# Kernel tuning notes

Hardware: AMD Instinct MI355X
Metric: run time of the kernel (lower is better)

## Reference

```python
import jax, jax.numpy as jnp
import numpy as np

# ---- hyperparams from init_kwargs ----
WX, WY, WW, WH = 10.0, 10.0, 5.0, 5.0      # bbox_reg_weights
BBOX_XFORM_CLIP = float(np.log(1000.0 / 16.0))
SCORE_THRESH = 0.05
NMS_THRESH = 0.5
DETECTIONS_PER_IMG = 100
MIN_SIZE = 0.01


def decode_boxes(rel_codes, boxes):
    # torchvision BoxCoder.decode_single with weights (10,10,5,5)
    widths = boxes[:, 2] - boxes[:, 0]
    heights = boxes[:, 3] - boxes[:, 1]
    ctr_x = boxes[:, 0] + 0.5 * widths
    ctr_y = boxes[:, 1] + 0.5 * heights
    dx = rel_codes[:, 0] / WX
    dy = rel_codes[:, 1] / WY
    dw = jnp.minimum(rel_codes[:, 2] / WW, BBOX_XFORM_CLIP)
    dh = jnp.minimum(rel_codes[:, 3] / WH, BBOX_XFORM_CLIP)
    pcx = dx * widths + ctr_x
    pcy = dy * heights + ctr_y
    pw = jnp.exp(dw) * widths
    ph = jnp.exp(dh) * heights
    return jnp.stack([pcx - 0.5 * pw, pcy - 0.5 * ph,
                      pcx + 0.5 * pw, pcy + 0.5 * ph], axis=1)


def iou_one_vs_all(box, boxes):
    # torchvision box_iou of one box vs all boxes -> [N]
    area1 = (box[2] - box[0]) * (box[3] - box[1])
    area2 = (boxes[:, 2] - boxes[:, 0]) * (boxes[:, 3] - boxes[:, 1])
    lt = jnp.maximum(box[:2], boxes[:, :2])
    rb = jnp.minimum(box[2:], boxes[:, 2:])
    wh = jnp.clip(rb - lt, 0.0)
    inter = wh[:, 0] * wh[:, 1]
    return inter / (area1 + area2 - inter)


def postprocess(class_logits, box_regression, proposals, image_h, image_w):
    boxes = decode_boxes(box_regression, proposals)            # [N,4]
    scores = jax.nn.softmax(class_logits, axis=-1)             # [N,C]
    # clip_boxes_to_image: x in [0,W], y in [0,H]
    boxes = jnp.stack([jnp.clip(boxes[:, 0], 0.0, image_w),
                       jnp.clip(boxes[:, 1], 0.0, image_h),
                       jnp.clip(boxes[:, 2], 0.0, image_w),
                       jnp.clip(boxes[:, 3], 0.0, image_h)], axis=1)
    # top-1 class per anchor (argmax over all classes, as in the source)
    labels = jnp.argmax(scores, axis=1)                        # [N]
    top1 = jnp.take_along_axis(scores, labels[:, None], axis=1)[:, 0]
    # score threshold + remove_small_boxes -> mask instead of dynamic filter
    valid = ((top1 > SCORE_THRESH)
             & ((boxes[:, 2] - boxes[:, 0]) >= MIN_SIZE)
             & ((boxes[:, 3] - boxes[:, 1]) >= MIN_SIZE))
    masked_scores = jnp.where(valid, top1, -1.0)

    # per-class (batched) NMS: pick max-score box, suppress same-class overlaps
    def step(s, _):
        idx = jnp.argmax(s)
        best_score = s[idx]
        best_box = boxes[idx]
        best_lab = labels[idx]
        sup = (iou_one_vs_all(best_box, boxes) > NMS_THRESH) & (labels == best_lab)
        s = jnp.where(sup, -1.0, s).at[idx].set(-1.0)
        return s, (best_box, best_score, best_lab)

    _, (out_b, out_s, out_l) = jax.lax.scan(step, masked_scores, None,
                                            length=DETECTIONS_PER_IMG)
    v = out_s > 0.0                                            # pad slots -> score<=0
    out_b = jnp.where(v[:, None], out_b, 0.0)
    out_s = jnp.where(v, out_s, 0.0)
    out_l = jnp.where(v, out_l, -1)
    return out_b, out_s, out_l


def setup_inputs() -> dict:
    key = jax.random.key(0)
    k1, k2, k3, k4, k5, k6 = jax.random.split(key, 6)
    N, C = 200000, 91
    H, W = 512, 512
    class_logits = jax.random.normal(k1, (N, C), dtype=jnp.float32)
    box_regression = jax.random.normal(k2, (N, 4), dtype=jnp.float32)
    cx = jax.random.uniform(k3, (N,), dtype=jnp.float32) * W
    cy = jax.random.uniform(k4, (N,), dtype=jnp.float32) * H
    bw = jax.random.uniform(k5, (N,), dtype=jnp.float32) * 120.0 + 8.0
    bh = jax.random.uniform(k6, (N,), dtype=jnp.float32) * 120.0 + 8.0
    proposals = jnp.stack([cx - 0.5 * bw, cy - 0.5 * bh,
                           cx + 0.5 * bw, cy + 0.5 * bh], axis=1)
    return {"class_logits": class_logits, "box_regression": box_regression,
            "proposals": proposals, "image_h": H, "image_w": W}


def reference(class_logits, box_regression, proposals, image_h, image_w):
    return postprocess(class_logits, box_regression, proposals,
                       float(image_h), float(image_w))
```

## Files before the change

### kernel.cpp

```cpp
#include <hip/hip_runtime.h>

#define NBINS   1024
#define TARGETC 192
#define CAPW    256
#define DET     100
#define XCLIP   4.135166556742356f
#define CHUNK   24
#define TILE4   576
#define K1GRID  2048
#define TOPK    8
#define NKEY    (K1GRID * TOPK)
#define SCAP    128

__device__ inline float scalar_to_float(const int* p) {
  int v = *p;
  return (v >= 0 && v < (1 << 20)) ? (float)v : __int_as_float(v);
}

struct Box { float x1, y1, x2, y2; };

__device__ inline Box decode_clip(float4 r, float4 p, float W, float H) {
  float w = p.z - p.x, h = p.w - p.y;
  float cx = p.x + 0.5f * w, cy = p.y + 0.5f * h;
  float dx = r.x / 10.f, dy = r.y / 10.f;
  float dw = fminf(r.z / 5.f, XCLIP), dh = fminf(r.w / 5.f, XCLIP);
  float pcx = dx * w + cx, pcy = dy * h + cy;
  float pw = __expf(dw) * w, ph = __expf(dh) * h;
  Box b;
  b.x1 = fminf(fmaxf(pcx - 0.5f * pw, 0.f), W);
  b.y1 = fminf(fmaxf(pcy - 0.5f * ph, 0.f), H);
  b.x2 = fminf(fmaxf(pcx + 0.5f * pw, 0.f), W);
  b.y2 = fminf(fmaxf(pcy + 0.5f * ph, 0.f), H);
  return b;
}

__global__ __launch_bounds__(256) void k1_score(
    const float* __restrict__ logits, const float* __restrict__ reg,
    const float* __restrict__ prop, const int* __restrict__ ph,
    const int* __restrict__ pw, unsigned long long* __restrict__ buckets,
    int N) {
  __shared__ float4 tile[2][TILE4];
  __shared__ unsigned long long candS[SCAP];
  __shared__ int candN;
  const int t = threadIdx.x, wv = t >> 6, lane = t & 63;
  if (t == 0) candN = 0;
  if (t < SCAP) candS[t] = 0ULL;
  const float W = scalar_to_float(pw), H = scalar_to_float(ph);
  const int nchunks = (N + CHUNK - 1) / CHUNK;

  auto stage = [&](int cc, int b) {
    const int rows = min(CHUNK, N - cc * CHUNK);
    const int nf = rows * 91, nf4 = nf >> 2;
    const float4* s4 = (const float4*)(logits + (size_t)cc * CHUNK * 91);
    float4* dst = &tile[b][0];
    #pragma unroll
    for (int k = 0; k < 3; ++k) {
      int b4 = (wv + (k << 2)) << 6;
      if (b4 < nf4) {
        int g = b4 + lane;
        if (g > nf4 - 1) g = nf4 - 1;
        __builtin_amdgcn_global_load_lds(
            (const __attribute__((address_space(1))) void*)(s4 + g),
            (__attribute__((address_space(3))) void*)(dst + b4),
            16, 0, 0);
      }
    }
    for (int i = (nf4 << 2) + t; i < nf; i += 256)
      ((float*)dst)[i] = logits[(size_t)cc * CHUNK * 91 + i];
  };

  int c = blockIdx.x;
  int cur = 0;
  if (c < nchunks) stage(c, 0);
  __syncthreads();
  while (c < nchunks) {
    const int cn = c + gridDim.x;
    if (cn < nchunks) stage(cn, cur ^ 1);
    const int rows = min(CHUNK, N - c * CHUNK);
    const int r = t >> 3, s = t & 7;
    if (r < rows) {
      const float* rowp = (const float*)&tile[cur][0] + r * 91;
      float mv = -3.402823466e38f; int mi = 1 << 20;
      float e0 = 0.f, e1 = 0.f;
      #pragma unroll
      for (int k = 0; k < 12; ++k) {
        int j = s + (k << 3);
        if (j < 91) {
          float v = rowp[j];
          float ex = __expf(v);
          if (k & 1) e1 += ex; else e0 += ex;
          if (v > mv) { mv = v; mi = j; }
        }
      }
      float e = e0 + e1;
      #pragma unroll
      for (int m = 1; m <= 4; m <<= 1) {
        float ov = __shfl_xor(mv, m, 64);
        int   oi = __shfl_xor(mi, m, 64);
        float oe = __shfl_xor(e, m, 64);
        e += oe;
        if (ov > mv || (ov == mv && oi < mi)) { mv = ov; mi = oi; }
      }
      if (s == 0) {
        float top1 = __expf(mv) / e;
        const int row = c * CHUNK + r;
        float4 rg = ((const float4*)reg)[row];
        float4 pp = ((const float4*)prop)[row];
        Box b = decode_clip(rg, pp, W, H);
        bool valid = (top1 > 0.05f) && ((b.x2 - b.x1) >= 0.01f) && ((b.y2 - b.y1) >= 0.01f);
        if (valid) {
          unsigned int low = ((0x1FFFFFFu - (unsigned int)row) << 7) |
                             (unsigned int)mi;
          unsigned long long key =
              ((unsigned long long)__float_as_uint(top1) << 32) |
              (unsigned long long)low;
          int pos = atomicAdd(&candN, 1);
          if (pos < SCAP) candS[pos] = key;
        }
      }
    }
    __syncthreads();
    cur ^= 1;
    c = cn;
  }
  __syncthreads();
  if (t < TOPK) buckets[(size_t)blockIdx.x * TOPK + t] = 0ULL;
  __syncthreads();
  if (t < SCAP) {
    unsigned long long my = candS[t];
    if (my != 0ULL) {
      int r = 0;
      #pragma unroll 8
      for (int j = 0; j < SCAP; ++j) r += (candS[j] > my) ? 1 : 0;
      if (r < TOPK) buckets[(size_t)blockIdx.x * TOPK + r] = my;
    }
  }
}

__global__ __launch_bounds__(1024) void k2_tail(
    const unsigned long long* __restrict__ buckets,
    const float* __restrict__ reg, const float* __restrict__ prop,
    const int* __restrict__ ph, const int* __restrict__ pw,
    float* __restrict__ out, int N) {
  __shared__ unsigned int lh[4][NBINS];
  __shared__ unsigned long long keys[CAPW];
  __shared__ unsigned int wsum[16];
  __shared__ unsigned int wtail[16];
  __shared__ int bstar;
  __shared__ unsigned int gcnt;
  __shared__ float rx1[CAPW], ry1[CAPW], rx2[CAPW], ry2[CAPW], rsc[CAPW];
  __shared__ int rlab[CAPW];
  __shared__ unsigned int sup[CAPW * 8];
  __shared__ unsigned int rowAny[8];
  __shared__ int keepL[DET];
  __shared__ int nkS;
  const int t = threadIdx.x;
  const int lane = t & 63, w = t >> 6;
  for (int i = t; i < 4 * NBINS; i += 1024) ((unsigned int*)lh)[i] = 0u;
  if (t < CAPW) keys[t] = 0ULL;
  if (t == 0) { bstar = 0; gcnt = 0u; nkS = 0; }
  __syncthreads();
  const ulonglong2* B2 = (const ulonglong2*)buckets;
  ulonglong2 v8[8];
  #pragma unroll
  for (int i = 0; i < 8; ++i) v8[i] = B2[t + (i << 10)];
  const int sh = t & 3;
  #pragma unroll
  for (int i = 0; i < 8; ++i) {
    if (v8[i].x) {
      float s = __uint_as_float((unsigned int)(v8[i].x >> 32));
      int b = (int)(s * (float)NBINS);
      if (b > NBINS - 1) b = NBINS - 1;
      atomicAdd(&lh[sh][b], 1u);
    }
    if (v8[i].y) {
      float s = __uint_as_float((unsigned int)(v8[i].y >> 32));
      int b = (int)(s * (float)NBINS);
      if (b > NBINS - 1) b = NBINS - 1;
      atomicAdd(&lh[sh][b], 1u);
    }
  }
  __syncthreads();
  const unsigned int h0 = lh[0][t] + lh[1][t] + lh[2][t] + lh[3][t];
  unsigned int v = h0;
  #pragma unroll
  for (int m = 1; m < 64; m <<= 1) {
    unsigned int o = __shfl_down(v, m, 64);
    if (lane + m < 64) v += o;
  }
  if (lane == 0) wsum[w] = v;
  __syncthreads();
  if (w == 0) {
    unsigned int u = (lane < 16) ? wsum[lane] : 0u;
    unsigned int inc = u;
    #pragma unroll
    for (int m = 1; m < 16; m <<= 1) {
      unsigned int o = __shfl_down(inc, m, 64);
      if (lane + m < 16) inc += o;
    }
    if (lane < 16) wtail[lane] = inc - u;
  }
  __syncthreads();
  const unsigned int St = v + wtail[w];
  const unsigned int St1 = St - h0;
  if (St >= TARGETC && St1 < TARGETC) {
    int b = (St > CAPW) ? t + 1 : t;
    if (b > NBINS - 1) b = NBINS - 1;
    bstar = b;
  }
  __syncthreads();
  const int bs = bstar;
  #pragma unroll
  for (int i = 0; i < 8; ++i) {
    #pragma unroll
    for (int e = 0; e < 2; ++e) {
      unsigned long long key = e ? v8[i].y : v8[i].x;
      if (key) {
        float s = __uint_as_float((unsigned int)(key >> 32));
        int b = (int)(s * (float)NBINS);
        if (b > NBINS - 1) b = NBINS - 1;
        if (b >= bs) {
          unsigned int pos = atomicAdd(&gcnt, 1u);
          if (pos < CAPW) keys[pos] = key;
        }
      }
    }
  }
  __syncthreads();
  const int count = (gcnt < (unsigned int)CAPW) ? (int)gcnt : CAPW;
  const float W = scalar_to_float(pw), H = scalar_to_float(ph);
  if (t < CAPW) {
    unsigned long long my = keys[t];
    int r = 0;
    #pragma unroll 8
    for (int j = 0; j < CAPW; ++j) r += (keys[j] > my) ? 1 : 0;
    if (t < count) {
      unsigned int low = (unsigned int)(my & 0xFFFFFFFFULL);
      int lab = (int)(low & 127u);
      int idx = (int)(0x1FFFFFFu - (low >> 7));
      if (idx < 0) idx = 0;
      if (idx > N - 1) idx = N - 1;
      float4 rr = ((const float4*)reg)[idx];
      float4 pp = ((const float4*)prop)[idx];
      Box b = decode_clip(rr, pp, W, H);
      rx1[r] = b.x1; ry1[r] = b.y1; rx2[r] = b.x2; ry2[r] = b.y2;
      rsc[r] = __uint_as_float((unsigned int)(my >> 32));
      rlab[r] = lab;
    } else {
      rlab[t] = -1 - t;
      rx1[t] = 0.f; ry1[t] = 0.f; rx2[t] = 0.f; ry2[t] = 0.f; rsc[t] = 0.f;
    }
  }
  sup[t] = 0u; sup[t + 1024] = 0u;
  if (t < 8) rowAny[t] = 0u;
  __syncthreads();
  #pragma unroll 4
  for (int p = t; p < (CAPW << 8); p += 1024) {
    int a = p >> 8, b = p & 255;
    if (a < b && rlab[a] == rlab[b]) {
      float ax = fmaxf(rx1[a], rx1[b]), ay = fmaxf(ry1[a], ry1[b]);
      float bx = fminf(rx2[a], rx2[b]), by = fminf(ry2[a], ry2[b]);
      float iw = fmaxf(bx - ax, 0.f), ih = fmaxf(by - ay, 0.f);
      float inter = iw * ih;
      float a1 = (rx2[a] - rx1[a]) * (ry2[a] - ry1[a]);
      float a2 = (rx2[b] - rx1[b]) * (ry2[b] - ry1[b]);
      if (inter / (a1 + a2 - inter) > 0.5f) {
        atomicOr(&sup[a * 8 + (b >> 5)], 1u << (b & 31));
        atomicOr(&rowAny[a >> 5], 1u << (a & 31));
      }
    }
  }
  __syncthreads();
  if (t == 0) {
    unsigned int m0 = 0, m1 = 0, m2 = 0, m3 = 0, m4 = 0, m5 = 0, m6 = 0, m7 = 0;
    int nk = 0;
#define RESOLVE_WORD(WI, MREG)                                          \
    if (nk < DET && (WI) * 32 < count) {                                \
      unsigned int anyw = rowAny[WI];                                   \
      int lim = count - (WI) * 32; if (lim > 32) lim = 32;              \
      for (int b = 0; b < lim; ++b) {                                   \
        if (nk >= DET) break;                                           \
        if (!((MREG >> b) & 1u)) {                                      \
          int p = (WI) * 32 + b;                                        \
          keepL[nk++] = p;                                              \
          if ((anyw >> b) & 1u) {                                       \
            const unsigned int* row = &sup[p * 8];                      \
            m0 |= row[0]; m1 |= row[1]; m2 |= row[2]; m3 |= row[3];     \
            m4 |= row[4]; m5 |= row[5]; m6 |= row[6]; m7 |= row[7];     \
          }                                                             \
        }                                                               \
      }                                                                 \
    }
    RESOLVE_WORD(0, m0)
    RESOLVE_WORD(1, m1)
    RESOLVE_WORD(2, m2)
    RESOLVE_WORD(3, m3)
    RESOLVE_WORD(4, m4)
    RESOLVE_WORD(5, m5)
    RESOLVE_WORD(6, m6)
    RESOLVE_WORD(7, m7)
#undef RESOLVE_WORD
    nkS = nk;
  }
  __syncthreads();
  if (t < DET) {
    int nk = nkS;
    bool vld = t < nk;
    int p = vld ? keepL[t] : 0;
    out[t * 4 + 0] = vld ? rx1[p] : 0.f;
    out[t * 4 + 1] = vld ? ry1[p] : 0.f;
    out[t * 4 + 2] = vld ? rx2[p] : 0.f;
    out[t * 4 + 3] = vld ? ry2[p] : 0.f;
    out[400 + t] = vld ? rsc[p] : 0.f;
    out[500 + t] = vld ? (float)rlab[p] : -1.f;
  }
}

extern "C" void kernel_launch(void* const* d_in, const int* in_sizes, int n_in,
                              void* d_out, int out_size, void* d_ws, size_t ws_size,
                              hipStream_t stream) {
  const float* logits = (const float*)d_in[0];
  const float* reg    = (const float*)d_in[1];
  const float* prop   = (const float*)d_in[2];
  const int*   ph     = (const int*)d_in[3];
  const int*   pw     = (const int*)d_in[4];
  float* out = (float*)d_out;

  const int N = in_sizes[1] / 4;

  unsigned long long* buckets = (unsigned long long*)d_ws;

  k1_score<<<K1GRID, 256, 0, stream>>>(logits, reg, prop, ph, pw, buckets, N);
  k2_tail<<<1, 1024, 0, stream>>>(buckets, reg, prop, ph, pw, out, N);
}
```

Measured before the change: 52.23 us.

## Add parallel segment top-k reduction stage before single-block tail kernel

Adds an intermediate kernel with 64 blocks, each reducing a 256-key segment of the per-block top-8 buckets to its top 32 by rank counting. The single-block tail kernel then reads only 2048 keys instead of 16384, shrinking its serial load and histogram work. The cost is an extra kernel launch and a second workspace buffer. It also assumes no segment holds more than 32 keys that belong in the final set.

```diff
diff --git a/kernel.cpp b/kernel.cpp
--- a/kernel.cpp
+++ b/kernel.cpp
@@ -11,6 +11,10 @@
 #define TOPK    8
 #define NKEY    (K1GRID * TOPK)
 #define SCAP    128
+#define SEG     64
+#define SEGKEYS (NKEY / SEG)
+#define TOP2    32
+#define NKEY2   (SEG * TOP2)
 
 __device__ inline float scalar_to_float(const int* p) {
   int v = *p;
@@ -137,8 +141,25 @@
   }
 }
 
+__global__ __launch_bounds__(256) void k2a_reduce(
+    const unsigned long long* __restrict__ buckets,
+    unsigned long long* __restrict__ slab2) {
+  __shared__ unsigned long long sk[SEGKEYS];
+  const int t = threadIdx.x, g = blockIdx.x;
+  unsigned long long my = buckets[(size_t)g * SEGKEYS + t];
+  sk[t] = my;
+  if (t < TOP2) slab2[g * TOP2 + t] = 0ULL;
+  __syncthreads();
+  if (my != 0ULL) {
+    int r = 0;
+    #pragma unroll 8
+    for (int j = 0; j < SEGKEYS; ++j) r += (sk[j] > my) ? 1 : 0;
+    if (r < TOP2) slab2[g * TOP2 + r] = my;
+  }
+}
+
 __global__ __launch_bounds__(1024) void k2_tail(
-    const unsigned long long* __restrict__ buckets,
+    const unsigned long long* __restrict__ slab2,
     const float* __restrict__ reg, const float* __restrict__ prop,
     const int* __restrict__ ph, const int* __restrict__ pw,
     float* __restrict__ out, int N) {
@@ -160,25 +181,19 @@
   if (t < CAPW) keys[t] = 0ULL;
   if (t == 0) { bstar = 0; gcnt = 0u; nkS = 0; }
   __syncthreads();
-  const ulonglong2* B2 = (const ulonglong2*)buckets;
-  ulonglong2 v8[8];
-  #pragma unroll
-  for (int i = 0; i < 8; ++i) v8[i] = B2[t + (i << 10)];
+  const ulonglong2 kk = ((const ulonglong2*)slab2)[t];
   const int sh = t & 3;
-  #pragma unroll
-  for (int i = 0; i < 8; ++i) {
-    if (v8[i].x) {
-      float s = __uint_as_float((unsigned int)(v8[i].x >> 32));
-      int b = (int)(s * (float)NBINS);
-      if (b > NBINS - 1) b = NBINS - 1;
-      atomicAdd(&lh[sh][b], 1u);
-    }
-    if (v8[i].y) {
-      float s = __uint_as_float((unsigned int)(v8[i].y >> 32));
-      int b = (int)(s * (float)NBINS);
-      if (b > NBINS - 1) b = NBINS - 1;
-      atomicAdd(&lh[sh][b], 1u);
-    }
+  if (kk.x) {
+    float s = __uint_as_float((unsigned int)(kk.x >> 32));
+    int b = (int)(s * (float)NBINS);
+    if (b > NBINS - 1) b = NBINS - 1;
+    atomicAdd(&lh[sh][b], 1u);
+  }
+  if (kk.y) {
+    float s = __uint_as_float((unsigned int)(kk.y >> 32));
+    int b = (int)(s * (float)NBINS);
+    if (b > NBINS - 1) b = NBINS - 1;
+    atomicAdd(&lh[sh][b], 1u);
   }
   __syncthreads();
   const unsigned int h0 = lh[0][t] + lh[1][t] + lh[2][t] + lh[3][t];
@@ -211,18 +226,15 @@
   __syncthreads();
   const int bs = bstar;
   #pragma unroll
-  for (int i = 0; i < 8; ++i) {
-    #pragma unroll
-    for (int e = 0; e < 2; ++e) {
-      unsigned long long key = e ? v8[i].y : v8[i].x;
-      if (key) {
-        float s = __uint_as_float((unsigned int)(key >> 32));
-        int b = (int)(s * (float)NBINS);
-        if (b > NBINS - 1) b = NBINS - 1;
-        if (b >= bs) {
-          unsigned int pos = atomicAdd(&gcnt, 1u);
-          if (pos < CAPW) keys[pos] = key;
-        }
+  for (int e = 0; e < 2; ++e) {
+    unsigned long long key = e ? kk.y : kk.x;
+    if (key) {
+      float s = __uint_as_float((unsigned int)(key >> 32));
+      int b = (int)(s * (float)NBINS);
+      if (b > NBINS - 1) b = NBINS - 1;
+      if (b >= bs) {
+        unsigned int pos = atomicAdd(&gcnt, 1u);
+        if (pos < CAPW) keys[pos] = key;
       }
     }
   }
@@ -328,8 +340,11 @@
 
   const int N = in_sizes[1] / 4;
 
-  unsigned long long* buckets = (unsigned long long*)d_ws;
+  char* ws = (char*)d_ws;
+  unsigned long long* buckets = (unsigned long long*)ws;
+  unsigned long long* slab2 = (unsigned long long*)(ws + NKEY * 8);
 
   k1_score<<<K1GRID, 256, 0, stream>>>(logits, reg, prop, ph, pw, buckets, N);
-  k2_tail<<<1, 1024, 0, stream>>>(buckets, reg, prop, ph, pw, out, N);
-}
+  k2a_reduce<<<SEG, 256, 0, stream>>>(buckets, slab2);
+  k2_tail<<<1, 1024, 0, stream>>>(slab2, reg, prop, ph, pw, out, N);
+}
```

New measurement: 54.20 us. +3.8%, slower.
